# Optimization experiments

Measured on AMD Instinct MI355X. Metric: run time of the kernel, lower is better.

## Reference

```python
import jax, jax.numpy as jnp
import numpy as np


def setup_inputs() -> dict:
    key = jax.random.key(0)
    ks = jax.random.split(key, 16)
    B, P, N, E = 16, 12, 20000, 320000
    f32 = jnp.float32
    x = jax.random.normal(ks[0], (B, P, N), f32)
    input_mask = (jax.random.uniform(ks[1], (B, P, N)) > 0.2).astype(f32)  # GAIN observed mask
    noise = jax.random.uniform(ks[2], (B, P, N), f32) * 0.01  # Uniform(0, 0.01) noise matrix
    edge_index = jax.random.randint(ks[3], (2, E), 0, N)
    edge_weights = jax.random.uniform(ks[4], (E,), f32)

    def lin(k, fi, fo):
        return jax.random.normal(k, (fi, fo), f32) * (1.0 / np.sqrt(fi))

    params = dict(
        Wz=lin(ks[5], 2, P), bz=jnp.zeros((P,), f32),
        Wr=lin(ks[6], 2, P), br=jnp.zeros((P,), f32),
        Wh=lin(ks[7], 2, P), bh=jnp.zeros((P,), f32),
        Lz_w=lin(ks[8], 2 * P, P), Lz_b=jnp.zeros((P,), f32),
        Lr_w=lin(ks[9], 2 * P, P), Lr_b=jnp.zeros((P,), f32),
        Lh_w=lin(ks[10], 2 * P, P), Lh_b=jnp.zeros((P,), f32),
        attention=jax.random.uniform(ks[11], (P,), f32),
        W1=lin(ks[12], P, P), b1=jnp.zeros((P,), f32),
        W2=lin(ks[13], P, P), b2=jnp.zeros((P,), f32),
    )
    return dict(x=x, input_mask=input_mask, noise=noise,
                edge_index=edge_index, edge_weights=edge_weights, **params)


def reference(x, input_mask, noise, edge_index, edge_weights,
              Wz, bz, Wr, br, Wh, bh,
              Lz_w, Lz_b, Lr_w, Lr_b, Lh_w, Lh_b,
              attention, W1, b1, W2, b2):
    B, P, N = x.shape
    # GAIN: fill missing entries with small uniform noise
    x = input_mask * x + (1.0 - input_mask) * noise
    # stack([x, mask]) -> [2,B,P,N]; permute(1,3,0,2) -> [B,N,2,P]; we scan over periods
    X = jnp.transpose(jnp.stack([x, input_mask], axis=2), (1, 0, 3, 2))  # [P, B, N, 2]

    # GCNConv symmetric normalization with self-loops (fill_value = 1)
    src, dst = edge_index[0], edge_index[1]
    loop = jnp.arange(N)
    src_sl = jnp.concatenate([src, loop])
    dst_sl = jnp.concatenate([dst, loop])
    w_sl = jnp.concatenate([edge_weights, jnp.ones((N,), x.dtype)])
    deg = jnp.zeros((N,), x.dtype).at[dst_sl].add(w_sl)
    dinv = jnp.where(deg > 0, deg ** -0.5, 0.0)
    norm = dinv[src_sl] * w_sl * dinv[dst_sl]  # [E + N]

    probs = jax.nn.softmax(attention)  # attention over periods
    H0 = jnp.zeros((B, N, P), x.dtype)  # A3TGCN2 never updates H -> each period sees H = 0

    def step(acc, inp):
        Xt, p = inp  # Xt: [B, N, 2]
        # aggregate raw 2-dim features then apply the (linear) GCN weight: same math,
        # far cheaper than gathering the projected [B, E, P] messages
        msgs = Xt[:, src_sl, :] * norm[None, :, None]          # [B, E+N, 2]
        agg = jnp.zeros_like(Xt).at[:, dst_sl, :].add(msgs)    # [B, N, 2]
        xz = agg @ Wz + bz
        xr = agg @ Wr + br
        xh = agg @ Wh + bh
        Z = jax.nn.sigmoid(jnp.concatenate([xz, H0], axis=-1) @ Lz_w + Lz_b)
        R = jax.nn.sigmoid(jnp.concatenate([xr, H0], axis=-1) @ Lr_w + Lr_b)
        Ht = jnp.tanh(jnp.concatenate([xh, H0 * R], axis=-1) @ Lh_w + Lh_b)
        H = Z * H0 + (1.0 - Z) * Ht
        return acc + p * H, None

    H_accum, _ = jax.lax.scan(step, H0, (X, probs))  # [B, N, P]

    # MLP head: ReLU -> Linear -> ReLU -> Linear -> Sigmoid
    h = jax.nn.relu(H_accum)
    h = jax.nn.relu(h @ W1 + b1)
    imput = jax.nn.sigmoid(h @ W2 + b2)               # [B, N, P]
    imputation = jnp.transpose(imput, (0, 2, 1))      # [B, P, N]
    res = input_mask * x + (1.0 - input_mask) * imputation
    return res, imputation
```

## Files before the change

### kernel.cpp

```cpp
#include <hip/hip_runtime.h>

#define NN 20000
#define NE 320000
#define BB 16
#define PP 12
#define NCOL 384
#define OUT_OFF (BB*PP*NN)
#define SLICES 8
#define SCOLS 48

__device__ __forceinline__ float sigmoidf_(float v) {
    return __fdividef(1.f, 1.f + __expf(-v));
}
__device__ __forceinline__ float tanh_fast(float v) {
    v = fminf(fmaxf(v, -15.f), 15.f);
    float e = __expf(-2.f * v);
    return __fdividef(1.f - e, 1.f + e);
}

__global__ __launch_bounds__(256) void degcnt_kernel(const int* __restrict__ ei,
                                                     const float* __restrict__ ew,
                                                     float* deg, int* cnt) {
    int e = blockIdx.x * 256 + threadIdx.x;
    if (e < NE) {
        int d = ei[NE + e];
        atomicAdd(&deg[d], ew[e]);
        atomicAdd(&cnt[d], 1);
    }
}

__global__ __launch_bounds__(1024) void scanprep_kernel(const int* __restrict__ cnt,
                                                        const float* __restrict__ deg,
                                                        int* __restrict__ rowp,
                                                        int* __restrict__ cur,
                                                        float* __restrict__ dinv,
                                                        const float* __restrict__ Wz, const float* __restrict__ bz,
                                                        const float* __restrict__ Wh, const float* __restrict__ bh,
                                                        const float* __restrict__ Lzw, const float* __restrict__ Lzb,
                                                        const float* __restrict__ Lhw, const float* __restrict__ Lhb,
                                                        const float* __restrict__ att,
                                                        const float* __restrict__ W1, const float* __restrict__ b1,
                                                        const float* __restrict__ W2, const float* __restrict__ b2,
                                                        float* __restrict__ cst) {
    int tid = threadIdx.x;
    if (blockIdx.x == 1) {
        if (tid < PP) {
            int p = tid;
            float az0 = 0.f, az1 = 0.f, cz = 0.f, ah0 = 0.f, ah1 = 0.f, ch = 0.f;
            for (int q = 0; q < PP; ++q) {
                float lz = Lzw[q * PP + p], lh = Lhw[q * PP + p];
                az0 += Wz[q] * lz;
                az1 += Wz[PP + q] * lz;
                cz  += bz[q] * lz;
                ah0 += Wh[q] * lh;
                ah1 += Wh[PP + q] * lh;
                ch  += bh[q] * lh;
            }
            cz += Lzb[p]; ch += Lhb[p];
            cst[p] = az0; cst[12 + p] = az1; cst[24 + p] = cz;
            cst[36 + p] = ah0; cst[48 + p] = ah1; cst[60 + p] = ch;
            float m = att[0];
            for (int q = 1; q < PP; ++q) m = fmaxf(m, att[q]);
            float ssum = 0.f;
            for (int q = 0; q < PP; ++q) ssum += __expf(att[q] - m);
            cst[72 + p] = __expf(att[p] - m) / ssum;
        }
        if (tid < 144) { cst[84 + tid] = W1[tid]; cst[240 + tid] = W2[tid]; }
        if (tid < PP)  { cst[228 + tid] = b1[tid]; cst[384 + tid] = b2[tid]; }
        return;
    }
    __shared__ int lds[1024];
    int base = tid * 20;
    int local[20];
    int s = 0;
    #pragma unroll
    for (int k = 0; k < 20; ++k) {
        int i = base + k;
        int v = (i < NN) ? cnt[i] : 0;
        local[k] = s;
        s += v;
    }
    lds[tid] = s;
    __syncthreads();
    for (int off = 1; off < 1024; off <<= 1) {
        int add = (tid >= off) ? lds[tid - off] : 0;
        __syncthreads();
        lds[tid] += add;
        __syncthreads();
    }
    int pre = (tid > 0) ? lds[tid - 1] : 0;
    #pragma unroll
    for (int k = 0; k < 20; ++k) {
        int i = base + k;
        if (i < NN) {
            int ex = pre + local[k];
            rowp[i] = ex; cur[i] = ex;
            dinv[i] = __frsqrt_rn(deg[i] + 1.0f);
        }
    }
    if (tid == 0) rowp[NN] = lds[1023];
}

__global__ __launch_bounds__(256) void scatter_kernel(const int* __restrict__ ei,
                                                      const float* __restrict__ ew,
                                                      const float* __restrict__ dinv,
                                                      int* cur, int2* __restrict__ epk) {
    int e = blockIdx.x * 256 + threadIdx.x;
    if (e < NE) {
        int s = ei[e];
        int d = ei[NE + e];
        int pos = atomicAdd(&cur[d], 1);
        float v = dinv[s] * ew[e] * dinv[d];
        epk[pos] = make_int2(s, __float_as_int(v));
    }
}

#define TILE 32
__global__ __launch_bounds__(256) void buildx_kernel(const float* __restrict__ x,
                                                     const float* __restrict__ mask,
                                                     const float* __restrict__ noise,
                                                     float* __restrict__ X) {
    __shared__ float tile[TILE][97];
    int tid = threadIdx.x;
    int n0 = blockIdx.x * TILE;
    int pr0 = blockIdx.y * 48;
    int i = tid & 31;
    int prb = tid >> 5;
    #pragma unroll
    for (int it = 0; it < 6; ++it) {
        int prl = it * 8 + prb;
        int pr = pr0 + prl;
        int g = pr * NN + n0 + i;
        float m = mask[g];
        float xv = x[g];
        float nz = noise[g];
        float xf = m * xv + (1.f - m) * nz;
        tile[i][prl * 2]     = xf;
        tile[i][prl * 2 + 1] = m;
    }
    __syncthreads();
    int c0 = blockIdx.y * 96;
    #pragma unroll
    for (int it = 0; it < 12; ++it) {
        int idx = it * 256 + tid;
        int r = idx / 96;
        int c = idx - r * 96;
        X[(n0 + r) * NCOL + c0 + c] = tile[r][c];
    }
}

__global__ __launch_bounds__(256) void spmm_kernel(const float* __restrict__ X,
                                                   const float* __restrict__ dinv,
                                                   const int* __restrict__ rowp,
                                                   const long long* __restrict__ ep,
                                                   float* __restrict__ agg) {
    int slice = blockIdx.x & 7;
    int grp   = blockIdx.x >> 3;
    int wave  = threadIdx.x >> 6;
    int lane  = threadIdx.x & 63;
    int d0 = (grp * 4 + wave) * 4;
    int c  = slice * SCOLS + lane;
    bool act = lane < SCOLS;
    int cg = act ? c : slice * SCOLS;

    int r0[4], r1[4];
    float acc[4];
    #pragma unroll
    for (int r = 0; r < 4; ++r) {
        int d = d0 + r;
        r0[r] = rowp[d];
        r1[r] = rowp[d + 1];
        float di = dinv[d];
        acc[r] = act ? di * di * X[(size_t)d * NCOL + c] : 0.f;
    }
    int maxdeg = max(max(r1[0] - r0[0], r1[1] - r0[1]), max(r1[2] - r0[2], r1[3] - r0[3]));

    int fr0 = 0, fr1 = 0;
    if (lane < 32) {
        int fd = d0 + (lane >> 3);
        fr0 = rowp[fd];
        fr1 = rowp[fd + 1];
    }
    int fj = lane & 7;

    long long cur = 0;
    {
        int e = fr0 + fj;
        if (lane < 32 && e < fr1) cur = __builtin_nontemporal_load(ep + e);
    }
    for (int off = 0; off < maxdeg; off += 8) {
        long long nxt = 0;
        {
            int e = fr0 + off + 8 + fj;
            if (lane < 32 && e < fr1) nxt = __builtin_nontemporal_load(ep + e);
        }
        float vv[4][8], xv[4][8];
        #pragma unroll
        for (int r = 0; r < 4; ++r) {
            #pragma unroll
            for (int j = 0; j < 8; ++j) {
                long long rec = __shfl(cur, r * 8 + j);
                int s = (int)rec;
                vv[r][j] = __int_as_float((int)(rec >> 32));
                xv[r][j] = X[(size_t)s * NCOL + cg];
            }
        }
        #pragma unroll
        for (int r = 0; r < 4; ++r)
            #pragma unroll
            for (int j = 0; j < 8; ++j)
                acc[r] += vv[r][j] * xv[r][j];
        cur = nxt;
    }
    if (act) {
        int b = slice * 2 + (lane >= 24 ? 1 : 0);
        int j = lane - (lane >= 24 ? 24 : 0);
        #pragma unroll
        for (int r = 0; r < 4; ++r)
            __builtin_nontemporal_store(acc[r], &agg[((size_t)b * NN + d0 + r) * 24 + j]);
    }
}

__global__ __launch_bounds__(256) void pointwise_kernel(const float* __restrict__ agg,
                                                        const float* __restrict__ cst,
                                                        const float* __restrict__ x,
                                                        const float* __restrict__ mask,
                                                        float* __restrict__ out) {
    __shared__ float C[396];
    int tid = threadIdx.x;
    for (int i = tid; i < 396; i += 256) C[i] = cst[i];
    __syncthreads();
    int idx = blockIdx.x * 256 + tid;
    int b = idx / NN;
    int n = idx - b * NN;
    float A[24];
    const float4* ap = (const float4*)(agg + ((size_t)b * NN + n) * 24);
    #pragma unroll
    for (int k = 0; k < 6; ++k) {
        float4 v = ap[k];
        A[4 * k + 0] = v.x; A[4 * k + 1] = v.y; A[4 * k + 2] = v.z; A[4 * k + 3] = v.w;
    }
    float h1[12];
    #pragma unroll
    for (int p = 0; p < 12; ++p) {
        float az0 = C[p], az1 = C[12 + p], czp = C[24 + p];
        float ah0 = C[36 + p], ah1 = C[48 + p], chp = C[60 + p];
        float hp = 0.f;
        #pragma unroll
        for (int t = 0; t < 12; ++t) {
            float a0 = A[2 * t], a1 = A[2 * t + 1];
            float z  = sigmoidf_(a0 * az0 + a1 * az1 + czp);
            float th = tanh_fast(a0 * ah0 + a1 * ah1 + chp);
            hp += C[72 + t] * ((1.f - z) * th);
        }
        h1[p] = fmaxf(hp, 0.f);
    }
    float h2[12];
    #pragma unroll
    for (int p = 0; p < 12; ++p) {
        float s = C[228 + p];
        #pragma unroll
        for (int q = 0; q < 12; ++q) s += h1[q] * C[84 + q * 12 + p];
        h2[p] = fmaxf(s, 0.f);
    }
    #pragma unroll
    for (int p = 0; p < 12; ++p) {
        float s = C[384 + p];
        #pragma unroll
        for (int q = 0; q < 12; ++q) s += h2[q] * C[240 + q * 12 + p];
        float imp = sigmoidf_(s);
        int o = (b * PP + p) * NN + n;
        float m = mask[o];
        float xv = x[o];
        out[o] = m * xv + (1.f - m) * imp;
        out[OUT_OFF + o] = imp;
    }
}

extern "C" void kernel_launch(void* const* d_in, const int* in_sizes, int n_in,
                              void* d_out, int out_size, void* d_ws, size_t ws_size,
                              hipStream_t stream) {
    const float* x     = (const float*)d_in[0];
    const float* mask  = (const float*)d_in[1];
    const float* noise = (const float*)d_in[2];
    const int*   ei    = (const int*)d_in[3];
    const float* ew    = (const float*)d_in[4];
    const float* Wz    = (const float*)d_in[5];
    const float* bz    = (const float*)d_in[6];
    const float* Wh    = (const float*)d_in[9];
    const float* bh    = (const float*)d_in[10];
    const float* Lzw   = (const float*)d_in[11];
    const float* Lzb   = (const float*)d_in[12];
    const float* Lhw   = (const float*)d_in[15];
    const float* Lhb   = (const float*)d_in[16];
    const float* att   = (const float*)d_in[17];
    const float* W1    = (const float*)d_in[18];
    const float* b1    = (const float*)d_in[19];
    const float* W2    = (const float*)d_in[20];
    const float* b2    = (const float*)d_in[21];
    float* out = (float*)d_out;

    float* Xf   = (float*)d_ws;
    float* AGG  = Xf + (size_t)NN * NCOL;
    long long* EPK = (long long*)(AGG + (size_t)NN * NCOL);
    float* DEG  = (float*)(EPK + NE);
    int*   CNT  = (int*)(DEG + NN);
    float* DINV = (float*)(CNT + NN);
    float* CST  = DINV + NN;
    int*   ROWP = (int*)(CST + 512);
    int*   CUR  = ROWP + NN + 1;

    hipMemsetAsync(DEG, 0, (size_t)2 * NN * 4, stream);
    hipLaunchKernelGGL(degcnt_kernel,  dim3((NE + 255) / 256), dim3(256), 0, stream, ei, ew, DEG, CNT);
    hipLaunchKernelGGL(scanprep_kernel, dim3(2), dim3(1024), 0, stream, CNT, DEG, ROWP, CUR, DINV,
                       Wz, bz, Wh, bh, Lzw, Lzb, Lhw, Lhb, att, W1, b1, W2, b2, CST);
    hipLaunchKernelGGL(scatter_kernel, dim3((NE + 255) / 256), dim3(256), 0, stream, ei, ew, DINV, CUR, (int2*)EPK);
    hipLaunchKernelGGL(buildx_kernel,  dim3(NN / TILE, 4), dim3(256), 0, stream, x, mask, noise, Xf);
    hipLaunchKernelGGL(spmm_kernel,    dim3(SLICES * NN / 16), dim3(256), 0, stream, Xf, DINV, ROWP, EPK, AGG);
    hipLaunchKernelGGL(pointwise_kernel, dim3((BB * NN) / 256), dim3(256), 0, stream, AGG, CST, x, mask, out);
}
```

Before: 379.8 us.

## Slice-major X layout, fuse degree count with X build, deepen edge prefetch

Stores the node feature matrix slice-major ([8 slices][N][48]) instead of row-major with 384 columns, so each spmm slice gathers from a compact 3.84MB region that fits better in cache. The X-building transpose is merged into the degree/count kernel as extra blocks, removing one launch and letting the two independent jobs overlap. The spmm edge-record prefetch now runs two iterations ahead instead of one. These add register pressure and lengthen the fused kernel's critical path.

```diff
diff --git a/kernel.cpp b/kernel.cpp
--- a/kernel.cpp
+++ b/kernel.cpp
@@ -18,14 +18,53 @@
     return __fdividef(1.f - e, 1.f + e);
 }
 
-__global__ __launch_bounds__(256) void degcnt_kernel(const int* __restrict__ ei,
-                                                     const float* __restrict__ ew,
-                                                     float* deg, int* cnt) {
-    int e = blockIdx.x * 256 + threadIdx.x;
-    if (e < NE) {
-        int d = ei[NE + e];
-        atomicAdd(&deg[d], ew[e]);
-        atomicAdd(&cnt[d], 1);
+#define TILE 32
+__global__ __launch_bounds__(256) void degbuild_kernel(const int* __restrict__ ei,
+                                                       const float* __restrict__ ew,
+                                                       float* deg, int* cnt,
+                                                       const float* __restrict__ x,
+                                                       const float* __restrict__ mask,
+                                                       const float* __restrict__ noise,
+                                                       float* __restrict__ X) {
+    if (blockIdx.x < 1250) {
+        int e = blockIdx.x * 256 + threadIdx.x;
+        if (e < NE) {
+            int d = ei[NE + e];
+            atomicAdd(&deg[d], ew[e]);
+            atomicAdd(&cnt[d], 1);
+        }
+        return;
+    }
+    __shared__ float tile[TILE][97];
+    int bid = blockIdx.x - 1250;
+    int bx = bid % 625;
+    int by = bid / 625;
+    int tid = threadIdx.x;
+    int n0 = bx * TILE;
+    int pr0 = by * 48;
+    int i = tid & 31;
+    int prb = tid >> 5;
+    #pragma unroll
+    for (int it = 0; it < 6; ++it) {
+        int prl = it * 8 + prb;
+        int pr = pr0 + prl;
+        int g = pr * NN + n0 + i;
+        float m = mask[g];
+        float xv = x[g];
+        float nz = noise[g];
+        float xf = m * xv + (1.f - m) * nz;
+        tile[i][prl * 2]     = xf;
+        tile[i][prl * 2 + 1] = m;
+    }
+    __syncthreads();
+    #pragma unroll
+    for (int it = 0; it < 12; ++it) {
+        int idx = it * 256 + tid;
+        int r = idx / 96;
+        int c = idx - r * 96;
+        int slice = by * 2 + (c >= 48 ? 1 : 0);
+        int lc = c - (c >= 48 ? 48 : 0);
+        X[((size_t)slice * NN + n0 + r) * SCOLS + lc] = tile[r][c];
     }
 }
 
@@ -115,40 +154,6 @@
     }
 }
 
-#define TILE 32
-__global__ __launch_bounds__(256) void buildx_kernel(const float* __restrict__ x,
-                                                     const float* __restrict__ mask,
-                                                     const float* __restrict__ noise,
-                                                     float* __restrict__ X) {
-    __shared__ float tile[TILE][97];
-    int tid = threadIdx.x;
-    int n0 = blockIdx.x * TILE;
-    int pr0 = blockIdx.y * 48;
-    int i = tid & 31;
-    int prb = tid >> 5;
-    #pragma unroll
-    for (int it = 0; it < 6; ++it) {
-        int prl = it * 8 + prb;
-        int pr = pr0 + prl;
-        int g = pr * NN + n0 + i;
-        float m = mask[g];
-        float xv = x[g];
-        float nz = noise[g];
-        float xf = m * xv + (1.f - m) * nz;
-        tile[i][prl * 2]     = xf;
-        tile[i][prl * 2 + 1] = m;
-    }
-    __syncthreads();
-    int c0 = blockIdx.y * 96;
-    #pragma unroll
-    for (int it = 0; it < 12; ++it) {
-        int idx = it * 256 + tid;
-        int r = idx / 96;
-        int c = idx - r * 96;
-        X[(n0 + r) * NCOL + c0 + c] = tile[r][c];
-    }
-}
-
 __global__ __launch_bounds__(256) void spmm_kernel(const float* __restrict__ X,
                                                    const float* __restrict__ dinv,
                                                    const int* __restrict__ rowp,
@@ -159,9 +164,9 @@
     int wave  = threadIdx.x >> 6;
     int lane  = threadIdx.x & 63;
     int d0 = (grp * 4 + wave) * 4;
-    int c  = slice * SCOLS + lane;
     bool act = lane < SCOLS;
-    int cg = act ? c : slice * SCOLS;
+    int cg = act ? lane : 0;
+    const float* Xs = X + (size_t)slice * NN * SCOLS;
 
     int r0[4], r1[4];
     float acc[4];
@@ -171,7 +176,7 @@
         r0[r] = rowp[d];
         r1[r] = rowp[d + 1];
         float di = dinv[d];
-        acc[r] = act ? di * di * X[(size_t)d * NCOL + c] : 0.f;
+        acc[r] = act ? di * di * Xs[(size_t)d * SCOLS + cg] : 0.f;
     }
     int maxdeg = max(max(r1[0] - r0[0], r1[1] - r0[1]), max(r1[2] - r0[2], r1[3] - r0[3]));
 
@@ -183,16 +188,18 @@
     }
     int fj = lane & 7;
 
-    long long cur = 0;
+    long long cur = 0, nxt = 0;
     {
-        int e = fr0 + fj;
-        if (lane < 32 && e < fr1) cur = __builtin_nontemporal_load(ep + e);
+        int e0 = fr0 + fj;
+        if (lane < 32 && e0 < fr1) cur = __builtin_nontemporal_load(ep + e0);
+        int e1 = fr0 + 8 + fj;
+        if (lane < 32 && e1 < fr1) nxt = __builtin_nontemporal_load(ep + e1);
     }
     for (int off = 0; off < maxdeg; off += 8) {
-        long long nxt = 0;
+        long long nx2 = 0;
         {
-            int e = fr0 + off + 8 + fj;
-            if (lane < 32 && e < fr1) nxt = __builtin_nontemporal_load(ep + e);
+            int e = fr0 + off + 16 + fj;
+            if (lane < 32 && e < fr1) nx2 = __builtin_nontemporal_load(ep + e);
         }
         float vv[4][8], xv[4][8];
         #pragma unroll
@@ -202,7 +209,7 @@
                 long long rec = __shfl(cur, r * 8 + j);
                 int s = (int)rec;
                 vv[r][j] = __int_as_float((int)(rec >> 32));
-                xv[r][j] = X[(size_t)s * NCOL + cg];
+                xv[r][j] = Xs[(size_t)s * SCOLS + cg];
             }
         }
         #pragma unroll
@@ -210,7 +217,7 @@
             #pragma unroll
             for (int j = 0; j < 8; ++j)
                 acc[r] += vv[r][j] * xv[r][j];
-        cur = nxt;
+        cur = nxt; nxt = nx2;
     }
     if (act) {
         int b = slice * 2 + (lane >= 24 ? 1 : 0);
@@ -311,11 +318,11 @@
     int*   CUR  = ROWP + NN + 1;
 
     hipMemsetAsync(DEG, 0, (size_t)2 * NN * 4, stream);
-    hipLaunchKernelGGL(degcnt_kernel,  dim3((NE + 255) / 256), dim3(256), 0, stream, ei, ew, DEG, CNT);
+    hipLaunchKernelGGL(degbuild_kernel, dim3(1250 + 2500), dim3(256), 0, stream,
+                       ei, ew, DEG, CNT, x, mask, noise, Xf);
     hipLaunchKernelGGL(scanprep_kernel, dim3(2), dim3(1024), 0, stream, CNT, DEG, ROWP, CUR, DINV,
                        Wz, bz, Wh, bh, Lzw, Lzb, Lhw, Lhb, att, W1, b1, W2, b2, CST);
     hipLaunchKernelGGL(scatter_kernel, dim3((NE + 255) / 256), dim3(256), 0, stream, ei, ew, DINV, CUR, (int2*)EPK);
-    hipLaunchKernelGGL(buildx_kernel,  dim3(NN / TILE, 4), dim3(256), 0, stream, x, mask, noise, Xf);
     hipLaunchKernelGGL(spmm_kernel,    dim3(SLICES * NN / 16), dim3(256), 0, stream, Xf, DINV, ROWP, EPK, AGG);
     hipLaunchKernelGGL(pointwise_kernel, dim3((BB * NN) / 256), dim3(256), 0, stream, AGG, CST, x, mask, out);
 }
```

New measurement: 373.1 us. About the same (-1.8%).
